# Performance work log

Hardware: AMD Instinct MI355X
Metric: run time of the kernel (lower is better)

Reference implementation:

```python
import jax, jax.numpy as jnp
import numpy as np

NUM_NODES = 9
HIDDEN = 512
BATCH = 8192
EPS = 1e-8


def _neighbor_lists(num_nodes):
    """Replicates torch.nonzero row-scan order: doubling, then complementary, then central."""
    doubling = {}
    for s, d in [(0, 1), (1, 3), (3, 7), (7, 6), (6, 4), (4, 0)]:
        if s < num_nodes and d < num_nodes:
            doubling.setdefault(d, []).append(s)
    comp = {}
    for a, b in [(0, 7), (1, 6), (3, 4), (2, 5)]:
        if a < num_nodes and b < num_nodes:
            comp.setdefault(a, []).append(b)
            comp.setdefault(b, []).append(a)
    nbrs = []
    for i in range(num_nodes):
        lst = sorted(doubling.get(i, [])) + sorted(comp.get(i, []))
        if num_nodes > 8:  # central hub node 8
            if i < 8:
                lst = lst + [8]
            elif i == 8:
                lst = lst + list(range(8))
        nbrs.append(lst)
    return nbrs


def _mobius_add(x, y, c):
    # x: (B,H) or broadcastable; Poincare-ball Mobius addition
    xy = jnp.sum(x * y, axis=-1, keepdims=True)
    xx = jnp.sum(x * x, axis=-1, keepdims=True)
    yy = jnp.sum(y * y, axis=-1, keepdims=True)
    num = (1 + 2 * c * xy + c * yy) * x + (1 - c * xx) * y
    den = 1 + 2 * c * xy + (c ** 2) * xx * yy
    return num / (den + EPS)


def setup_inputs() -> dict:
    key = jax.random.key(0)
    k0, k1, k2, k3 = jax.random.split(key, 4)
    node_features = jax.random.normal(k0, (BATCH, NUM_NODES, HIDDEN), jnp.float32)
    bound = 1.0 / np.sqrt(HIDDEN)
    to_w = jax.random.uniform(k1, (HIDDEN, HIDDEN), jnp.float32, -bound, bound)
    to_b = jnp.zeros((HIDDEN,), jnp.float32)
    from_w = jax.random.uniform(k2, (HIDDEN, HIDDEN), jnp.float32, -bound, bound)
    from_b = jnp.zeros((HIDDEN,), jnp.float32)
    # kaiming_normal with tanh gain 5/3; fan_in of (N,N,H) tensor = N*H
    std = (5.0 / 3.0) / np.sqrt(NUM_NODES * HIDDEN)
    mobius_weights = jax.random.normal(k3, (NUM_NODES, NUM_NODES, HIDDEN), jnp.float32) * std
    curvature = jnp.asarray(-1.0, jnp.float32)
    return {
        "node_features": node_features,
        "curvature": curvature,
        "to_w": to_w,
        "to_b": to_b,
        "from_w": from_w,
        "from_b": from_b,
        "mobius_weights": mobius_weights,
    }


def reference(node_features, curvature, to_w, to_b, from_w, from_b, mobius_weights):
    c = jnp.abs(curvature)
    # to_poincare_ball
    x_proj = node_features @ to_w.T + to_b                      # (B,N,H)
    norm = jnp.linalg.norm(x_proj, axis=-1, keepdims=True)
    h = jnp.tanh(norm) * x_proj / (norm + EPS)                  # (B,N,H)

    nbrs = _neighbor_lists(NUM_NODES)
    cols = []
    for i in range(NUM_NODES):  # tiny fixed structural loop (9 nodes)
        r = h[:, i]                                             # (B,H)
        for j in nbrs[i]:       # sequential (non-commutative) Mobius fold
            t = _mobius_add(h[:, j], mobius_weights[i, j][None, :], c)
            r = _mobius_add(r, t, c)
        cols.append(r)
    result = jnp.stack(cols, axis=1)                            # (B,N,H)

    # from_poincare_ball
    return result @ from_w.T + from_b
```

## Files before the change

kernel.cpp:

```cpp
#include <hip/hip_runtime.h>

typedef unsigned short u16;
typedef unsigned int u32;
typedef __bf16 bf16x8 __attribute__((ext_vector_type(8)));
typedef float floatx4 __attribute__((ext_vector_type(4)));

#define EPSF 1e-8f

__device__ float g_nrm[81];

__device__ __forceinline__ float bf2f(u16 u) { return __uint_as_float(((u32)u) << 16); }
__device__ __forceinline__ u16 f2bf(float f) {
  u32 u = __float_as_uint(f);
  u += 0x7fffu + ((u >> 16) & 1u);
  return (u16)(u >> 16);
}
__device__ __forceinline__ void unpack2(u32 u, float& a, float& b) {
  a = __uint_as_float(u << 16);
  b = __uint_as_float(u & 0xffff0000u);
}
__device__ __forceinline__ float wave_sum(float s) {
#pragma unroll
  for (int m = 32; m; m >>= 1) s += __shfl_xor(s, m, 64);
  return s;
}
__device__ __forceinline__ u32 cvtpk(float lo, float hi) {
  u32 r;
  asm("v_cvt_pk_bf16_f32 %0, %1, %2" : "=v"(r) : "v"(lo), "v"(hi));
  return r;
}
__device__ __forceinline__ float rcp(float x) { return __builtin_amdgcn_rcpf(x); }
__device__ __forceinline__ float tanh_pos(float x) {
  float e = __builtin_amdgcn_exp2f(x * 2.885390081777927f);
  return __builtin_fmaf(-2.f, rcp(e + 1.f), 1.f);
}

typedef __attribute__((address_space(1))) void gv_t;
typedef __attribute__((address_space(3))) void lv_t;
__device__ __forceinline__ void gload_lds16(const u16* g, u16* l) {
  __builtin_amdgcn_global_load_lds((const gv_t*)g, (lv_t*)l, 16, 0, 0);
}

__device__ __forceinline__ bool sniff_f32(const void* curv) {
  return ((const u16*)curv)[0] == 0;
}
__device__ __forceinline__ uint4 load8bf(const void* base, size_t off, bool isf32) {
  if (!isf32) return *(const uint4*)((const u16*)base + off);
  const float* p = (const float*)base + off;
  float4 a = *(const float4*)p;
  float4 b = *(const float4*)(p + 4);
  uint4 r;
  r.x = (u32)f2bf(a.x) | ((u32)f2bf(a.y) << 16);
  r.y = (u32)f2bf(a.z) | ((u32)f2bf(a.w) << 16);
  r.z = (u32)f2bf(b.x) | ((u32)f2bf(b.y) << 16);
  r.w = (u32)f2bf(b.z) | ((u32)f2bf(b.w) << 16);
  return r;
}
__device__ __forceinline__ void load8f(const void* base, size_t off, bool isf32, float* o) {
  if (isf32) {
    const float* p = (const float*)base + off;
    float4 a = *(const float4*)p;
    float4 b = *(const float4*)(p + 4);
    o[0] = a.x; o[1] = a.y; o[2] = a.z; o[3] = a.w;
    o[4] = b.x; o[5] = b.y; o[6] = b.z; o[7] = b.w;
  } else {
    const u16* p = (const u16*)base + off;
    uint4 r = *(const uint4*)p;
    unpack2(r.x, o[0], o[1]);
    unpack2(r.y, o[2], o[3]);
    unpack2(r.z, o[4], o[5]);
    unpack2(r.w, o[6], o[7]);
  }
}

__global__ __launch_bounds__(64) void mwnorm(const void* __restrict__ MW,
                                             const void* __restrict__ curv) {
  const bool f32 = sniff_f32(curv);
  const int e = blockIdx.x;
  const int lane = threadIdx.x;
  float y[8];
  load8f(MW, (size_t)e * 512 + lane * 8, f32, y);
  float s = 0.f;
#pragma unroll
  for (int p = 0; p < 8; p++) s += y[p] * y[p];
  s = wave_sum(s);
  if (lane == 0) g_nrm[e] = s;
}

__global__ __launch_bounds__(256) void cvt_kernel(
    const float* __restrict__ A, const float* __restrict__ TW, const float* __restrict__ FW,
    u16* __restrict__ oA, u16* __restrict__ oTW, u16* __restrict__ oFW,
    const void* __restrict__ curv)
{
  if (!sniff_f32(curv)) return;
  const long CA = 37748736L / 8;
  const long CW = 262144L / 8;
  const long total = CA + 2 * CW;
  for (long i = (long)blockIdx.x * blockDim.x + threadIdx.x; i < total;
       i += (long)gridDim.x * blockDim.x) {
    const float* s; u16* d; long j;
    if (i < CA)           { s = A;  d = oA;  j = i; }
    else if (i < CA + CW) { s = TW; d = oTW; j = i - CA; }
    else                  { s = FW; d = oFW; j = i - CA - CW; }
    float4 a = *(const float4*)(s + j * 8);
    float4 b = *(const float4*)(s + j * 8 + 4);
    uint4 o;
    o.x = cvtpk(a.x, a.y);
    o.y = cvtpk(a.z, a.w);
    o.z = cvtpk(b.x, b.y);
    o.w = cvtpk(b.z, b.w);
    *(uint4*)(d + j * 8) = o;
  }
}

template <int FINAL>
__global__ __launch_bounds__(256) void gemm_fast(
    const void* __restrict__ origA, const u16* __restrict__ convA,
    const void* __restrict__ origB, const u16* __restrict__ convB,
    const void* __restrict__ bias, void* __restrict__ out,
    const void* __restrict__ curv, int M, int N, int K)
{
  __shared__ __align__(16) u16 As[128 * 32];
  __shared__ __align__(16) u16 Bs[128 * 32];

  const bool f32 = sniff_f32(curv);
  const u16* A = f32 ? convA : (const u16*)origA;
  const u16* B = f32 ? convB : (const u16*)origB;

  const int t = threadIdx.x;
  const int lane = t & 63;
  const int w = t >> 6;
  const int waveM = w >> 1, waveN = w & 1;

  int lid = blockIdx.x + blockIdx.y * gridDim.x;
  const int nwg = gridDim.x * gridDim.y;
  if ((nwg & 7) == 0) lid = (lid & 7) * (nwg >> 3) + (lid >> 3);
  const int m0 = (lid / gridDim.x) * 128;
  const int n0 = (lid % gridDim.x) * 128;

  floatx4 acc[4][4];
#pragma unroll
  for (int i = 0; i < 4; i++)
#pragma unroll
    for (int j = 0; j < 4; j++) {
      acc[i][j][0] = 0.f; acc[i][j][1] = 0.f;
      acc[i][j][2] = 0.f; acc[i][j][3] = 0.f;
    }

  const u16* ga0 = A + (size_t)(m0 + (t >> 2)) * K + (t & 3) * 8;
  const u16* ga1 = ga0 + (size_t)64 * K;
  const u16* gb0 = B + (size_t)(n0 + (t >> 2)) * K + (t & 3) * 8;
  const u16* gb1 = gb0 + (size_t)64 * K;
  u16* lA0 = As + w * 512;
  u16* lA1 = As + 2048 + w * 512;
  u16* lB0 = Bs + w * 512;
  u16* lB1 = Bs + 2048 + w * 512;

  const int am = waveM * 64 + (lane & 15);
  const int bn = waveN * 64 + (lane & 15);
  const int kq = (lane >> 4) * 8;

  for (int k0 = 0; k0 < K; k0 += 32) {
    gload_lds16(ga0 + k0, lA0);
    gload_lds16(ga1 + k0, lA1);
    gload_lds16(gb0 + k0, lB0);
    gload_lds16(gb1 + k0, lB1);
    __syncthreads();

    bf16x8 af[4], bfr[4];
#pragma unroll
    for (int mt = 0; mt < 4; mt++)
      af[mt] = *(const bf16x8*)(As + (am + mt * 16) * 32 + kq);
#pragma unroll
    for (int nt = 0; nt < 4; nt++)
      bfr[nt] = *(const bf16x8*)(Bs + (bn + nt * 16) * 32 + kq);
#pragma unroll
    for (int mt = 0; mt < 4; mt++)
#pragma unroll
      for (int nt = 0; nt < 4; nt++)
        acc[mt][nt] = __builtin_amdgcn_mfma_f32_16x16x32_bf16(af[mt], bfr[nt], acc[mt][nt], 0, 0, 0);
    __syncthreads();
  }

  const int quad = lane >> 4;
  const int cl = lane & 15;
#pragma unroll
  for (int mt = 0; mt < 4; mt++)
#pragma unroll
    for (int nt = 0; nt < 4; nt++) {
      const int col = n0 + waveN * 64 + nt * 16 + cl;
      const float bs = f32 ? ((const float*)bias)[col] : bf2f(((const u16*)bias)[col]);
#pragma unroll
      for (int r = 0; r < 4; r++) {
        const int row = m0 + waveM * 64 + mt * 16 + quad * 4 + r;
        const float v = acc[mt][nt][r] + bs;
        if (FINAL && f32) ((float*)out)[(size_t)row * N + col] = v;
        else              ((u16*)out)[(size_t)row * N + col] = f2bf(v);
      }
    }
}

__global__ __launch_bounds__(256) void mobius4(
    u16* Xf, u16* Xb, const void* __restrict__ MW, const void* __restrict__ curv)
{
  __shared__ float h[9][512];
  __shared__ float hh[9];
  __shared__ float chh[9];
  __shared__ float b1n[9];

  const bool f32 = sniff_f32(curv);
  u16* X = f32 ? Xf : Xb;

  const int b = blockIdx.x;
  const int t = threadIdx.x;
  const int lane = t & 63;
  const int w = t >> 6;
  const float c = f32 ? fabsf(((const float*)curv)[0]) : fabsf(bf2f(((const u16*)curv)[0]));
  const float c2 = 2.f * c;

  for (int r = w; r < 9; r += 4) {
    uint4 raw = *(const uint4*)(X + ((size_t)b * 9 + r) * 512 + lane * 8);
    float x[8];
    unpack2(raw.x, x[0], x[1]);
    unpack2(raw.y, x[2], x[3]);
    unpack2(raw.z, x[4], x[5]);
    unpack2(raw.w, x[6], x[7]);
    float s = 0.f;
#pragma unroll
    for (int p = 0; p < 8; p++) s += x[p] * x[p];
    s = wave_sum(s);
    const float norm = sqrtf(s);
    const float scale = tanh_pos(norm) * rcp(norm + EPSF);
#pragma unroll
    for (int p = 0; p < 8; p++) h[r][lane * 8 + p] = x[p] * scale;
    if (lane == 0) {
      const float q = scale * scale * s;
      hh[r] = q;
      chh[r] = c * q;
      b1n[r] = 1.f - c * q;
    }
  }
  __syncthreads();

  const int baseNode[4] = {8, 0, 3, 6};
  const int cntNode[4] = {1, 3, 3, 2};
  const int nbrCnt[9] = {3, 3, 2, 3, 3, 2, 3, 3, 8};
  const int nbrTab[9][8] = {
      {4, 7, 8, 0, 0, 0, 0, 0}, {0, 6, 8, 0, 0, 0, 0, 0}, {5, 8, 0, 0, 0, 0, 0, 0},
      {1, 4, 8, 0, 0, 0, 0, 0}, {6, 3, 8, 0, 0, 0, 0, 0}, {2, 8, 0, 0, 0, 0, 0, 0},
      {7, 1, 8, 0, 0, 0, 0, 0}, {3, 0, 8, 0, 0, 0, 0, 0}, {0, 1, 2, 3, 4, 5, 6, 7}};

  for (int s = 0; s < cntNode[w]; s++) {
    const int i = baseNode[w] + s;
    float r8[8];
#pragma unroll
    for (int p = 0; p < 8; p++) r8[p] = h[i][lane * 8 + p];
    float rr = hh[i];

    for (int e = 0; e < nbrCnt[i]; e++) {
      const int j = nbrTab[i][e];
      float y[8];
      load8f(MW, ((size_t)i * 9 + j) * 512 + lane * 8, f32, y);
      float x8[8];
#pragma unroll
      for (int p = 0; p < 8; p++) x8[p] = h[j][lane * 8 + p];

      float xy = 0.f;
#pragma unroll
      for (int p = 0; p < 8; p++) xy = __builtin_fmaf(x8[p], y[p], xy);
      xy = wave_sum(xy);

      const float xx = hh[j];
      const float yy = g_nrm[i * 9 + j];
      const float cyy = c * yy;
      const float a1 = __builtin_fmaf(c2, xy, 1.f + cyy);
      const float b1 = b1n[j];
      const float d1 = __builtin_fmaf(chh[j], cyy, 1.f + EPSF);
      const float inv1 = rcp(__builtin_fmaf(c2, xy, d1));

      float z8[8];
#pragma unroll
      for (int p = 0; p < 8; p++) z8[p] = __builtin_fmaf(a1, x8[p], b1 * y[p]);

      float rz = 0.f;
#pragma unroll
      for (int p = 0; p < 8; p++) rz = __builtin_fmaf(r8[p], z8[p], rz);
      rz = wave_sum(rz);

      const float rt = inv1 * rz;
      const float a1b1 = a1 * b1;
      const float inv1sq = inv1 * inv1;
      float ttn = __builtin_fmaf(b1 * b1, yy, __builtin_fmaf(a1b1 + a1b1, xy, a1 * a1 * xx));
      const float tt = ttn * inv1sq;

      const float ctt = c * tt;
      const float crr = c * rr;
      const float a2 = __builtin_fmaf(c2, rt, 1.f + ctt);
      const float b2 = 1.f - crr;
      const float d2 = __builtin_fmaf(crr, ctt, 1.f + EPSF);
      const float inv2 = rcp(__builtin_fmaf(c2, rt, d2));
      const float ca = a2 * inv2;
      const float cz = b2 * inv2 * inv1;
#pragma unroll
      for (int p = 0; p < 8; p++)
        r8[p] = __builtin_fmaf(ca, r8[p], cz * z8[p]);
      const float a2b2 = a2 * b2;
      const float inv2sq = inv2 * inv2;
      rr = inv2sq * __builtin_fmaf(b2 * b2, tt,
                    __builtin_fmaf(a2b2 + a2b2, rt, a2 * a2 * rr));
    }

    uint4 o;
    o.x = cvtpk(r8[0], r8[1]);
    o.y = cvtpk(r8[2], r8[3]);
    o.z = cvtpk(r8[4], r8[5]);
    o.w = cvtpk(r8[6], r8[7]);
    *(uint4*)(X + ((size_t)b * 9 + i) * 512 + lane * 8) = o;
  }
}

__global__ __launch_bounds__(256) void gemm1_bt_bias(
    const void* __restrict__ A, const void* __restrict__ Bw,
    const void* __restrict__ bias, void* out, void* ws,
    const void* __restrict__ curv, int M, int N, int K)
{
  __shared__ __align__(16) u16 As[128 * 32];
  __shared__ __align__(16) u16 Bs[128 * 32];

  const bool f32 = sniff_f32(curv);
  u16* C = f32 ? (u16*)ws : (u16*)out;

  const int t = threadIdx.x;
  const int lane = t & 63;
  const int w = t >> 6;
  const int waveM = w >> 1, waveN = w & 1;
  const int m0 = blockIdx.y * 128;
  const int n0 = blockIdx.x * 128;

  floatx4 acc[4][4];
#pragma unroll
  for (int i = 0; i < 4; i++)
#pragma unroll
    for (int j = 0; j < 4; j++) {
      acc[i][j][0] = 0.f; acc[i][j][1] = 0.f;
      acc[i][j][2] = 0.f; acc[i][j][3] = 0.f;
    }

  const int r0 = t >> 2;
  const int c0 = (t & 3) * 8;
  const size_t oa0 = (size_t)(m0 + r0) * K + c0;
  const size_t oa1 = (size_t)(m0 + 64 + r0) * K + c0;
  const size_t ob0 = (size_t)(n0 + r0) * K + c0;
  const size_t ob1 = (size_t)(n0 + 64 + r0) * K + c0;

  for (int k0 = 0; k0 < K; k0 += 32) {
    uint4 a0 = load8bf(A, oa0 + k0, f32);
    uint4 a1 = load8bf(A, oa1 + k0, f32);
    uint4 b0 = load8bf(Bw, ob0 + k0, f32);
    uint4 b1 = load8bf(Bw, ob1 + k0, f32);
    __syncthreads();
    *(uint4*)(As + t * 8) = a0;
    *(uint4*)(As + 2048 + t * 8) = a1;
    *(uint4*)(Bs + t * 8) = b0;
    *(uint4*)(Bs + 2048 + t * 8) = b1;
    __syncthreads();

    bf16x8 af[4], bfr[4];
    const int am = waveM * 64 + (lane & 15);
    const int bn = waveN * 64 + (lane & 15);
    const int kq = (lane >> 4) * 8;
#pragma unroll
    for (int mt = 0; mt < 4; mt++)
      af[mt] = *(const bf16x8*)(As + (am + mt * 16) * 32 + kq);
#pragma unroll
    for (int nt = 0; nt < 4; nt++)
      bfr[nt] = *(const bf16x8*)(Bs + (bn + nt * 16) * 32 + kq);
#pragma unroll
    for (int mt = 0; mt < 4; mt++)
#pragma unroll
      for (int nt = 0; nt < 4; nt++)
        acc[mt][nt] = __builtin_amdgcn_mfma_f32_16x16x32_bf16(af[mt], bfr[nt], acc[mt][nt], 0, 0, 0);
  }

  const int quad = lane >> 4;
  const int cl = lane & 15;
#pragma unroll
  for (int mt = 0; mt < 4; mt++)
#pragma unroll
    for (int nt = 0; nt < 4; nt++) {
      const int col = n0 + waveN * 64 + nt * 16 + cl;
      const float bs = f32 ? ((const float*)bias)[col] : bf2f(((const u16*)bias)[col]);
#pragma unroll
      for (int r = 0; r < 4; r++) {
        const int row = m0 + waveM * 64 + mt * 16 + quad * 4 + r;
        C[(size_t)row * N + col] = f2bf(acc[mt][nt][r] + bs);
      }
    }
}

__global__ __launch_bounds__(256) void gemm2_fullN(
    const void* __restrict__ Bw, const void* __restrict__ bias,
    void* out, void* ws, const void* __restrict__ curv,
    int M, int N, int K)
{
  __shared__ __align__(16) u16 As[32 * 32];
  __shared__ __align__(16) u16 Bs[512 * 32];

  const bool f32 = sniff_f32(curv);
  const u16* A = f32 ? (const u16*)ws : (const u16*)out;

  const int t = threadIdx.x;
  const int lane = t & 63;
  const int w = t >> 6;
  const int m0 = blockIdx.x * 32;

  floatx4 acc[2][8];
#pragma unroll
  for (int i = 0; i < 2; i++)
#pragma unroll
    for (int j = 0; j < 8; j++) {
      acc[i][j][0] = 0.f; acc[i][j][1] = 0.f;
      acc[i][j][2] = 0.f; acc[i][j][3] = 0.f;
    }

  const int r0 = t >> 2;
  const int c0 = (t & 3) * 8;

  for (int k0 = 0; k0 < K; k0 += 32) {
    uint4 av = make_uint4(0, 0, 0, 0);
    if (t < 128)
      av = *(const uint4*)(A + (size_t)(m0 + r0) * K + k0 + c0);
    uint4 bv[8];
#pragma unroll
    for (int q = 0; q < 8; q++)
      bv[q] = load8bf(Bw, (size_t)(q * 64 + r0) * K + k0 + c0, f32);
    __syncthreads();
    if (t < 128) *(uint4*)(As + t * 8) = av;
#pragma unroll
    for (int q = 0; q < 8; q++)
      *(uint4*)(Bs + q * 2048 + t * 8) = bv[q];
    __syncthreads();

    bf16x8 af[2], bfr[8];
    const int ml = lane & 15;
    const int kq = (lane >> 4) * 8;
#pragma unroll
    for (int mt = 0; mt < 2; mt++)
      af[mt] = *(const bf16x8*)(As + (mt * 16 + ml) * 32 + kq);
#pragma unroll
    for (int nt = 0; nt < 8; nt++)
      bfr[nt] = *(const bf16x8*)(Bs + (w * 128 + nt * 16 + ml) * 32 + kq);
#pragma unroll
    for (int mt = 0; mt < 2; mt++)
#pragma unroll
      for (int nt = 0; nt < 8; nt++)
        acc[mt][nt] = __builtin_amdgcn_mfma_f32_16x16x32_bf16(af[mt], bfr[nt], acc[mt][nt], 0, 0, 0);
  }

  const int quad = lane >> 4;
  const int cl = lane & 15;
#pragma unroll
  for (int mt = 0; mt < 2; mt++)
#pragma unroll
    for (int nt = 0; nt < 8; nt++) {
      const int col = w * 128 + nt * 16 + cl;
      const float bs = f32 ? ((const float*)bias)[col] : bf2f(((const u16*)bias)[col]);
#pragma unroll
      for (int r = 0; r < 4; r++) {
        const int row = m0 + mt * 16 + quad * 4 + r;
        const float v = acc[mt][nt][r] + bs;
        if (f32) ((float*)out)[(size_t)row * N + col] = v;
        else     ((u16*)out)[(size_t)row * N + col] = f2bf(v);
      }
    }
}

extern "C" void kernel_launch(void* const* d_in, const int* in_sizes, int n_in,
                              void* d_out, int out_size, void* d_ws, size_t ws_size,
                              hipStream_t stream) {
  const void* nf = d_in[0];
  const void* curv = d_in[1];
  const void* to_w = d_in[2];
  const void* to_b = d_in[3];
  const void* fr_w = d_in[4];
  const void* fr_b = d_in[5];
  const void* mw = d_in[6];

  const int M = 8192 * 9, N = 512, K = 512;
  const size_t XB = (size_t)M * N * 2;
  const size_t WWB = (size_t)512 * 512 * 2;

  u16 *xb = nullptr, *a_bf = nullptr, *tw_bf = nullptr, *fw_bf = nullptr;
  bool fast = false;
  if (ws_size >= 2 * XB + 2 * WWB) {
    xb    = (u16*)d_ws;
    a_bf  = (u16*)((char*)d_ws + XB);
    tw_bf = (u16*)((char*)d_ws + 2 * XB);
    fw_bf = (u16*)((char*)d_ws + 2 * XB + WWB);
    fast = true;
  } else if (ws_size >= XB + 2 * WWB) {
    xb    = (u16*)d_ws;
    tw_bf = (u16*)((char*)d_ws + XB);
    fw_bf = (u16*)((char*)d_ws + XB + WWB);
    a_bf  = (u16*)d_out;
    fast = true;
  } else if (ws_size >= XB + WWB) {
    xb    = (u16*)d_ws;
    fw_bf = (u16*)((char*)d_ws + XB);
    a_bf  = (u16*)d_out;
    tw_bf = (u16*)((char*)d_out + XB);
    fast = true;
  }

  mwnorm<<<81, 64, 0, stream>>>(mw, curv);

  if (fast) {
    cvt_kernel<<<2048, 256, 0, stream>>>((const float*)nf, (const float*)to_w,
                                         (const float*)fr_w, a_bf, tw_bf, fw_bf, curv);
    gemm_fast<0><<<dim3(N / 128, M / 128), 256, 0, stream>>>(
        nf, a_bf, to_w, tw_bf, to_b, xb, curv, M, N, K);
    mobius4<<<8192, 256, 0, stream>>>(xb, xb, mw, curv);
    gemm_fast<1><<<dim3(N / 128, M / 128), 256, 0, stream>>>(
        xb, xb, fr_w, fw_bf, fr_b, d_out, curv, M, N, K);
  } else {
    gemm1_bt_bias<<<dim3(N / 128, M / 128), 256, 0, stream>>>(nf, to_w, to_b, d_out, d_ws, curv, M, N, K);
    mobius4<<<8192, 256, 0, stream>>>((u16*)d_ws, (u16*)d_out, mw, curv);
    gemm2_fullN<<<M / 32, 256, 0, stream>>>(fr_w, fr_b, d_out, d_ws, curv, M, N, K);
  }
}
```

Baseline: 454.2 us.

## Fuse fp32-to-bf16 conversion of node features into first GEMM's A-tile staging

The separate pass that converted the whole 151MB fp32 node-feature tensor to bf16 in workspace is removed. The first GEMM now reads fp32 A directly, converts it in registers and writes bf16 into LDS. A small kernel still converts only the two weight matrices. This removes a full write and reread of the converted activations. In exchange, A-tile loads become synchronous register round trips instead of direct global-to-LDS loads, and fp32 A is reread once per N-tile (four times).

```diff
diff --git a/kernel.cpp b/kernel.cpp
--- a/kernel.cpp
+++ b/kernel.cpp
@@ -87,33 +87,27 @@
   if (lane == 0) g_nrm[e] = s;
 }
 
-__global__ __launch_bounds__(256) void cvt_kernel(
-    const float* __restrict__ A, const float* __restrict__ TW, const float* __restrict__ FW,
-    u16* __restrict__ oA, u16* __restrict__ oTW, u16* __restrict__ oFW,
-    const void* __restrict__ curv)
+__global__ __launch_bounds__(256) void cvt_w(
+    const float* __restrict__ TW, const float* __restrict__ FW,
+    u16* __restrict__ oTW, u16* __restrict__ oFW, const void* __restrict__ curv)
 {
   if (!sniff_f32(curv)) return;
-  const long CA = 37748736L / 8;
-  const long CW = 262144L / 8;
-  const long total = CA + 2 * CW;
-  for (long i = (long)blockIdx.x * blockDim.x + threadIdx.x; i < total;
-       i += (long)gridDim.x * blockDim.x) {
-    const float* s; u16* d; long j;
-    if (i < CA)           { s = A;  d = oA;  j = i; }
-    else if (i < CA + CW) { s = TW; d = oTW; j = i - CA; }
-    else                  { s = FW; d = oFW; j = i - CA - CW; }
-    float4 a = *(const float4*)(s + j * 8);
-    float4 b = *(const float4*)(s + j * 8 + 4);
-    uint4 o;
-    o.x = cvtpk(a.x, a.y);
-    o.y = cvtpk(a.z, a.w);
-    o.z = cvtpk(b.x, b.y);
-    o.w = cvtpk(b.z, b.w);
-    *(uint4*)(d + j * 8) = o;
-  }
-}
-
-template <int FINAL>
+  const int i = blockIdx.x * 256 + threadIdx.x;
+  const bool first = i < 32768;
+  const float* s = first ? TW : FW;
+  u16* d = first ? oTW : oFW;
+  const long j = first ? i : i - 32768;
+  float4 a = *(const float4*)(s + j * 8);
+  float4 b = *(const float4*)(s + j * 8 + 4);
+  uint4 o;
+  o.x = cvtpk(a.x, a.y);
+  o.y = cvtpk(a.z, a.w);
+  o.z = cvtpk(b.x, b.y);
+  o.w = cvtpk(b.z, b.w);
+  *(uint4*)(d + j * 8) = o;
+}
+
+template <int FINAL, int CONVA>
 __global__ __launch_bounds__(256) void gemm_fast(
     const void* __restrict__ origA, const u16* __restrict__ convA,
     const void* __restrict__ origB, const u16* __restrict__ convB,
@@ -124,8 +118,10 @@
   __shared__ __align__(16) u16 Bs[128 * 32];
 
   const bool f32 = sniff_f32(curv);
+  const bool stageA32 = CONVA && f32;
   const u16* A = f32 ? convA : (const u16*)origA;
   const u16* B = f32 ? convB : (const u16*)origB;
+  const float* Af = (const float*)origA;
 
   const int t = threadIdx.x;
   const int lane = t & 63;
@@ -147,24 +143,44 @@
       acc[i][j][2] = 0.f; acc[i][j][3] = 0.f;
     }
 
-  const u16* ga0 = A + (size_t)(m0 + (t >> 2)) * K + (t & 3) * 8;
+  const int r0 = t >> 2;
+  const int c0 = (t & 3) * 8;
+  const u16* ga0 = A + (size_t)(m0 + r0) * K + c0;
   const u16* ga1 = ga0 + (size_t)64 * K;
-  const u16* gb0 = B + (size_t)(n0 + (t >> 2)) * K + (t & 3) * 8;
+  const u16* gb0 = B + (size_t)(n0 + r0) * K + c0;
   const u16* gb1 = gb0 + (size_t)64 * K;
+  const float* fa0 = Af + (size_t)(m0 + r0) * K + c0;
+  const float* fa1 = fa0 + (size_t)64 * K;
   u16* lA0 = As + w * 512;
   u16* lA1 = As + 2048 + w * 512;
   u16* lB0 = Bs + w * 512;
   u16* lB1 = Bs + 2048 + w * 512;
+  u16* wA0 = As + t * 8;
+  u16* wA1 = As + 2048 + t * 8;
 
   const int am = waveM * 64 + (lane & 15);
   const int bn = waveN * 64 + (lane & 15);
   const int kq = (lane >> 4) * 8;
 
   for (int k0 = 0; k0 < K; k0 += 32) {
-    gload_lds16(ga0 + k0, lA0);
-    gload_lds16(ga1 + k0, lA1);
     gload_lds16(gb0 + k0, lB0);
     gload_lds16(gb1 + k0, lB1);
+    if (stageA32) {
+      float4 a0 = *(const float4*)(fa0 + k0);
+      float4 a1 = *(const float4*)(fa0 + k0 + 4);
+      float4 b0 = *(const float4*)(fa1 + k0);
+      float4 b1 = *(const float4*)(fa1 + k0 + 4);
+      uint4 o0, o1;
+      o0.x = cvtpk(a0.x, a0.y); o0.y = cvtpk(a0.z, a0.w);
+      o0.z = cvtpk(a1.x, a1.y); o0.w = cvtpk(a1.z, a1.w);
+      o1.x = cvtpk(b0.x, b0.y); o1.y = cvtpk(b0.z, b0.w);
+      o1.z = cvtpk(b1.x, b1.y); o1.w = cvtpk(b1.z, b1.w);
+      *(uint4*)wA0 = o0;
+      *(uint4*)wA1 = o1;
+    } else {
+      gload_lds16(ga0 + k0, lA0);
+      gload_lds16(ga1 + k0, lA1);
+    }
     __syncthreads();
 
     bf16x8 af[4], bfr[4];
@@ -490,24 +506,16 @@
   const size_t XB = (size_t)M * N * 2;
   const size_t WWB = (size_t)512 * 512 * 2;
 
-  u16 *xb = nullptr, *a_bf = nullptr, *tw_bf = nullptr, *fw_bf = nullptr;
+  u16 *xb = nullptr, *tw_bf = nullptr, *fw_bf = nullptr;
   bool fast = false;
-  if (ws_size >= 2 * XB + 2 * WWB) {
-    xb    = (u16*)d_ws;
-    a_bf  = (u16*)((char*)d_ws + XB);
-    tw_bf = (u16*)((char*)d_ws + 2 * XB);
-    fw_bf = (u16*)((char*)d_ws + 2 * XB + WWB);
-    fast = true;
-  } else if (ws_size >= XB + 2 * WWB) {
+  if (ws_size >= XB + 2 * WWB) {
     xb    = (u16*)d_ws;
     tw_bf = (u16*)((char*)d_ws + XB);
     fw_bf = (u16*)((char*)d_ws + XB + WWB);
-    a_bf  = (u16*)d_out;
     fast = true;
   } else if (ws_size >= XB + WWB) {
     xb    = (u16*)d_ws;
     fw_bf = (u16*)((char*)d_ws + XB);
-    a_bf  = (u16*)d_out;
     tw_bf = (u16*)((char*)d_out + XB);
     fast = true;
   }
@@ -515,12 +523,12 @@
   mwnorm<<<81, 64, 0, stream>>>(mw, curv);
 
   if (fast) {
-    cvt_kernel<<<2048, 256, 0, stream>>>((const float*)nf, (const float*)to_w,
-                                         (const float*)fr_w, a_bf, tw_bf, fw_bf, curv);
-    gemm_fast<0><<<dim3(N / 128, M / 128), 256, 0, stream>>>(
-        nf, a_bf, to_w, tw_bf, to_b, xb, curv, M, N, K);
+    cvt_w<<<256, 256, 0, stream>>>((const float*)to_w, (const float*)fr_w,
+                                   tw_bf, fw_bf, curv);
+    gemm_fast<0, 1><<<dim3(N / 128, M / 128), 256, 0, stream>>>(
+        nf, (const u16*)nf, to_w, tw_bf, to_b, xb, curv, M, N, K);
     mobius4<<<8192, 256, 0, stream>>>(xb, xb, mw, curv);
-    gemm_fast<1><<<dim3(N / 128, M / 128), 256, 0, stream>>>(
+    gemm_fast<1, 0><<<dim3(N / 128, M / 128), 256, 0, stream>>>(
         xb, xb, fr_w, fw_bf, fr_b, d_out, curv, M, N, K);
   } else {
     gemm1_bt_bias<<<dim3(N / 128, M / 128), 256, 0, stream>>>(nf, to_w, to_b, d_out, d_ws, curv, M, N, K);
```

New measurement: 443.6 us. 1.02x faster.
